# Performance work log

Measured on AMD Instinct MI355X. Metric: run time of the kernel, lower is better.

## Reference

```python
import jax, jax.numpy as jnp
import numpy as np

SPIRAL_LEN = 12
V_LEVELS = [32768, 8192, 2048, 512, 128]
CHANNELS = [3, 32, 64, 128, 256]


def spiral_conv(x, spiral, W, b):
    # x: [B, V, C_in]; spiral: [V, S] neighbor indices
    B, V, C = x.shape
    g = x[:, spiral, :]                      # [B, V, S, C_in] irregular gather
    g = g.reshape(B, V, -1)                  # [B, V, S*C_in]
    return g @ W + b                         # [B, V, C_out]


def mesh_pool(x, idx, w):
    # sparse down_transform (<=3 nnz per row): out[b,i,:] = sum_k w[i,k] * x[b, idx[i,k], :]
    return jnp.einsum('bvkc,vk->bvc', x[:, idx, :], w)


def setup_inputs() -> dict:
    key = jax.random.key(0)
    ks = jax.random.split(key, 32)
    S = SPIRAL_LEN
    V = V_LEVELS
    C = CHANNELS
    d = {}
    d['x'] = jax.random.normal(ks[0], (32, V[0], C[0]), dtype=jnp.float32)
    for i in range(4):
        d[f'spiral{i}'] = jax.random.randint(ks[1 + i], (V[i], S), 0, V[i])
        d[f'didx{i}'] = jax.random.randint(ks[5 + i], (V[i + 1], 3), 0, V[i])
        w = jax.random.uniform(ks[9 + i], (V[i + 1], 3), dtype=jnp.float32)
        d[f'dw{i}'] = w / w.sum(-1, keepdims=True)  # barycentric-like rows
        fan_in = S * C[i]
        d[f'W{i}'] = jax.random.normal(ks[13 + i], (fan_in, C[i + 1]), dtype=jnp.float32) * np.float32(1.0 / np.sqrt(fan_in))
        d[f'b{i}'] = jnp.zeros((C[i + 1],), jnp.float32)
    flat_in = V[4] * C[4]  # num_vert * out_channels[-2]
    d['Wl1'] = jax.random.normal(ks[20], (flat_in, 512), dtype=jnp.float32) * np.float32(1.0 / np.sqrt(flat_in))
    d['bl1'] = jnp.zeros((512,), jnp.float32)
    d['Wl2'] = jax.random.normal(ks[21], (512, 64), dtype=jnp.float32) * np.float32(1.0 / np.sqrt(512))
    d['bl2'] = jnp.zeros((64,), jnp.float32)
    return d


def reference(x, spiral0, spiral1, spiral2, spiral3,
              didx0, didx1, didx2, didx3,
              dw0, dw1, dw2, dw3,
              W0, b0, W1, b1, W2, b2, W3, b3,
              Wl1, bl1, Wl2, bl2):
    spirals = (spiral0, spiral1, spiral2, spiral3)
    didx = (didx0, didx1, didx2, didx3)
    dw = (dw0, dw1, dw2, dw3)
    Wb = ((W0, b0), (W1, b1), (W2, b2), (W3, b3))
    for i in range(4):  # SpiralEnblock: elu(spiral_conv(x)) -> sparse pool
        x = jax.nn.elu(spiral_conv(x, spirals[i], *Wb[i]))
        x = mesh_pool(x, didx[i], dw[i])
    B = x.shape[0]
    x = x.reshape(B, -1)                     # [B, num_vert * C_last]
    x = jax.nn.elu(x @ Wl1 + bl1)            # [B, 512]
    y = x @ Wl2 + bl2                        # [B, latent]
    return (x, y)
```

## Files before the change

### kernel.cpp

```cpp
#include <hip/hip_runtime.h>
#include <cstdint>
#include <cstddef>

typedef _Float16 f16x8 __attribute__((ext_vector_type(8)));
typedef _Float16 f16x4 __attribute__((ext_vector_type(4)));
typedef float f32x4 __attribute__((ext_vector_type(4)));

static __device__ __forceinline__ float elu_f(float t) {
    return t > 0.0f ? t : expm1f(t);
}

typedef __attribute__((address_space(1))) const unsigned int guint;
typedef __attribute__((address_space(3))) unsigned int       luint;
static __device__ __forceinline__ void gload_lds16(const void* g, void* l)
{
    __builtin_amdgcn_global_load_lds((guint*)g, (luint*)l, 16, 0, 0);
}

template<int N>
static __device__ __forceinline__ void vm_wait()
{
    static_assert(N == 0 || N == 4 || N == 5, "vmcnt literal");
    if constexpr (N == 0)      asm volatile("s_waitcnt vmcnt(0)" ::: "memory");
    else if constexpr (N == 4) asm volatile("s_waitcnt vmcnt(4)" ::: "memory");
    else                       asm volatile("s_waitcnt vmcnt(5)" ::: "memory");
    __builtin_amdgcn_sched_barrier(0);
}

static __device__ __forceinline__ int block_pu0(int bid, int P, int vshift_out, int nbl)
{
    if (nbl < 0) return bid * P;
    int xcd  = bid & 7;
    int slot = bid >> 3;
    int nb   = slot & ((1 << nbl) - 1);
    int tile = slot >> nbl;
    return ((xcd + (nb << 3)) << vshift_out) + tile * P;
}

template<int KTOT, int C_OUT, int BN>
__global__ __launch_bounds__(256)
void prep_w(const float* __restrict__ W, _Float16* __restrict__ o)
{
    constexpr int KT = KTOT/64;
    int i = blockIdx.x * 256 + threadIdx.x;
    if (i >= KTOT*C_OUT) return;
    int j = i & 7;
    int rest = i >> 3;
    int n = rest % BN;
    int kc = (rest / BN) & 7;
    int t = (rest / (BN*8)) % KT;
    int y = rest / (BN*8*KT);
    int k = t*64 + kc*8 + j;
    o[i] = (_Float16)W[(size_t)k*C_OUT + y*BN + n];
}

__global__ __launch_bounds__(256)
void prep_w0(const float* __restrict__ W, _Float16* __restrict__ o)
{
    int i = blockIdx.x * 256 + threadIdx.x;
    if (i >= 2048) return;
    int j = i & 7;
    int n = (i >> 3) & 31;
    int kc = i >> 8;
    int k = kc*8 + j;
    int s = k >> 2, c = k & 3;
    float v = (s < 12 && c < 3) ? W[(size_t)(s*3 + c)*32 + n] : 0.0f;
    o[i] = (_Float16)v;
}

__global__ __launch_bounds__(256)
void prep_xT(const float* __restrict__ x, _Float16* __restrict__ xT)
{
    __shared__ _Float16 t[16][64*4 + 8];
    const int v0 = blockIdx.x * 64;
    const int tid = threadIdx.x;
    #pragma unroll
    for (int it = 0; it < 4; ++it) {
        int e = it*256 + tid;
        int b = e >> 6, v = e & 63;
        const float* p = x + ((size_t)b*32768 + v0 + v)*3;
        f16x4 h;
        h[0] = (_Float16)p[0]; h[1] = (_Float16)p[1];
        h[2] = (_Float16)p[2]; h[3] = (_Float16)0.f;
        *(f16x4*)&t[b][v*4] = h;
    }
    __syncthreads();
    #pragma unroll
    for (int it = 0; it < 2; ++it) {
        int e = it*256 + tid;
        int vl = e >> 3, s = e & 7;
        f16x4 a = *(const f16x4*)&t[2*s][vl*4];
        f16x4 b = *(const f16x4*)&t[2*s+1][vl*4];
        f16x8 h;
        h[0]=a[0]; h[1]=a[1]; h[2]=a[2]; h[3]=a[3];
        h[4]=b[0]; h[5]=b[1]; h[6]=b[2]; h[7]=b[3];
        *(f16x8*)&xT[((size_t)(v0+vl)*16 + s*2)*4] = h;
    }
}

__global__ __launch_bounds__(256)
void prep_gidx(const int* __restrict__ didx, const int* __restrict__ spiral,
               unsigned int* __restrict__ g)
{
    int i = blockIdx.x*256 + threadIdx.x;
    if (i >= 24576*8) return;
    int q = i & 7;
    int row = i >> 3;
    unsigned int val = 0;
    if (q < 6) {
        int v = didx[row];
        unsigned int s0 = (unsigned int)spiral[v*12 + q*2];
        unsigned int s1 = (unsigned int)spiral[v*12 + q*2 + 1];
        val = s0 | (s1 << 16);
    }
    g[i] = val;
}

__global__ __launch_bounds__(256)
void conv0T(const _Float16* __restrict__ xT, const unsigned int* __restrict__ gidx,
            const _Float16* __restrict__ Wp, const float* __restrict__ bias,
            const float* __restrict__ dwt, _Float16* __restrict__ out)
{
    __shared__ _Float16 Ep[4][512];
    const int tid  = threadIdx.x;
    const int wave = tid >> 6;
    const int lane = tid & 63;
    const int quad = lane >> 4;
    const int l16  = lane & 15;
    const int u0   = blockIdx.x * 8 + wave * 2;

    f16x8 bf[2][2];
    #pragma unroll
    for (int kt = 0; kt < 2; ++kt)
        #pragma unroll
        for (int nt = 0; nt < 2; ++nt)
            bf[kt][nt] = *(const f16x8*)&Wp[(((kt*4+quad)*32) + nt*16 + l16)*8];
    float bv[2] = { bias[l16], bias[16 + l16] };

    #pragma unroll
    for (int ui = 0; ui < 2; ++ui) {
        int u = u0 + ui;
        f32x4 pacc[2] = {{0.f,0.f,0.f,0.f},{0.f,0.f,0.f,0.f}};
        #pragma unroll
        for (int kp = 0; kp < 3; ++kp) {
            int r = u*3 + kp;
            unsigned int gp0 = gidx[r*8 + quad];
            unsigned int gp1 = gidx[r*8 + 4 + quad];
            f16x4 a0 = *(const f16x4*)&xT[(size_t)(gp0 & 0xffffu)*64 + l16*4];
            f16x4 a1 = *(const f16x4*)&xT[(size_t)(gp0 >> 16)*64 + l16*4];
            f16x4 a2 = *(const f16x4*)&xT[(size_t)(gp1 & 0xffffu)*64 + l16*4];
            f16x4 a3 = *(const f16x4*)&xT[(size_t)(gp1 >> 16)*64 + l16*4];
            f16x8 af0, af1;
            af0[0]=a0[0]; af0[1]=a0[1]; af0[2]=a0[2]; af0[3]=a0[3];
            af0[4]=a1[0]; af0[5]=a1[1]; af0[6]=a1[2]; af0[7]=a1[3];
            af1[0]=a2[0]; af1[1]=a2[1]; af1[2]=a2[2]; af1[3]=a2[3];
            af1[4]=a3[0]; af1[5]=a3[1]; af1[6]=a3[2]; af1[7]=a3[3];
            float dw = dwt[r];
            #pragma unroll
            for (int nt = 0; nt < 2; ++nt) {
                f32x4 m = {0.f,0.f,0.f,0.f};
                m = __builtin_amdgcn_mfma_f32_16x16x32_f16(af0, bf[0][nt], m, 0,0,0);
                m = __builtin_amdgcn_mfma_f32_16x16x32_f16(af1, bf[1][nt], m, 0,0,0);
                #pragma unroll
                for (int rr = 0; rr < 4; ++rr)
                    pacc[nt][rr] += dw * elu_f(m[rr] + bv[nt]);
            }
        }
        #pragma unroll
        for (int nt = 0; nt < 2; ++nt)
            #pragma unroll
            for (int rr = 0; rr < 4; ++rr)
                Ep[wave][(quad*4+rr)*32 + nt*16 + l16] = (_Float16)pacc[nt][rr];
        int b  = lane >> 2;
        int c8 = lane & 3;
        f16x8 rowv = *(const f16x8*)&Ep[wave][b*32 + c8*8];
        *(f16x8*)&out[(size_t)b*262144 + (size_t)u*32 + c8*8] = rowv;
    }
}

template<int C_IN, int C_OUT, int P, int BN, int WGM, int WGN, bool OUT_HALF>
__global__ __launch_bounds__(256)
void conv_pool_mfma(const _Float16* __restrict__ x, const int* __restrict__ spiral,
                    const _Float16* __restrict__ Wp, const float* __restrict__ bias,
                    const int* __restrict__ didx, const float* __restrict__ dwt,
                    void* __restrict__ outv, int vshift_in, int vshift_out, int nbl)
{
    constexpr int R    = 3*P;
    constexpr int KTOT = 12*C_IN;
    constexpr int KT   = KTOT/64;
    constexpr int NST  = KT*2;
    constexpr int WTM  = R/WGM;
    constexpr int WTN  = BN/WGN;
    constexpr int NMT  = WTM/16;
    constexpr int NNT  = WTN/16;
    constexpr int C4   = BN/4;
    constexpr int GS   = (C_IN == 32) ? 1 : 2;
    constexpr int NG   = NST / GS;
    constexpr int CPR  = GS * 4;
    constexpr int CPRS = (CPR == 4) ? 2 : 3;
    constexpr int ACH  = R * CPR;
    constexpr int BCH  = GS * BN * 4;
    constexpr int AIPW = ACH / 256;
    constexpr int BIPW = BCH / 256;
    constexpr int LPW  = AIPW + BIPW;
    constexpr int NBUF = 3;
    constexpr int ASUBH = R * GS * 32;
    constexpr int BSUBH = GS * 32 * BN;
    static_assert(WTM % 16 == 0 && WTN % 16 == 0, "tile");
    static_assert(R <= 256 && (P*C4) % 256 == 0, "loops");
    static_assert(ACH % 256 == 0 && BCH % 256 == 0, "stage");
    static_assert(NST % GS == 0 && GS*32 <= C_IN, "group");
    static_assert(NG >= 3, "pipeline depth");

    constexpr size_t BUFB = (size_t)(NBUF*(ASUBH + BSUBH)) * 2;
    constexpr size_t EB   = (size_t)R * (BN + 4) * 2;
    constexpr size_t GOFF = (BUFB > EB ? BUFB : EB);
    static_assert(GOFF + (size_t)R*12*2 <= 65536, "LDS budget");
    __shared__ __align__(16) char smem[GOFF + (size_t)R*12*2];
    _Float16* Ab = (_Float16*)smem;
    _Float16* Bb = (_Float16*)(smem + (size_t)NBUF*ASUBH*2);
    unsigned short* gidx = (unsigned short*)(smem + GOFF);
    _Float16* E = (_Float16*)smem;

    const int tid  = threadIdx.x;
    const int wave = tid >> 6;
    const int lane = tid & 63;
    const int quad = lane >> 4;
    const int l16  = lane & 15;
    const int wm   = wave / WGN;
    const int wn   = wave % WGN;
    const int pu0  = block_pu0(blockIdx.x, P, vshift_out, nbl);
    const int n0   = blockIdx.y * BN;
    const int vmask_out = (1 << vshift_out) - 1;
    const int base_in = (pu0 >> vshift_out) << vshift_in;

    if (tid < R) {
        int ul = tid / 3;
        int kp = tid - ul*3;
        int u  = (pu0 + ul) & vmask_out;
        int v  = didx[u*3 + kp];
        const int* svp = spiral + v*12;
        #pragma unroll
        for (int j = 0; j < 12; ++j) gidx[tid*12 + j] = (unsigned short)svp[j];
    }
    __syncthreads();

    f32x4 acc[NMT][NNT];
    #pragma unroll
    for (int i = 0; i < NMT; ++i)
        #pragma unroll
        for (int j = 0; j < NNT; ++j) acc[i][j] = (f32x4){0.f, 0.f, 0.f, 0.f};

    const _Float16* xb = x + (size_t)base_in * C_IN;

    auto SWZ = [](int r) -> int {
        return (CPR == 4) ? ((r & 3) ^ ((r >> 2) & 3)) : (r & 7);
    };

    auto stage = [&](int g, int buf) {
        const int k0g = g * GS * 32;
        const int sv  = k0g / C_IN;
        const int c0  = k0g % C_IN;
        _Float16* Ad = Ab + (size_t)buf * ASUBH;
        #pragma unroll
        for (int i = 0; i < AIPW; ++i) {
            int t  = (wave*AIPW + i)*64 + lane;
            int r  = t >> CPRS;
            int q  = t & (CPR - 1);
            int qq = q ^ SWZ(r);
            int gr = gidx[r*12 + sv];
            gload_lds16(xb + (size_t)gr*C_IN + c0 + qq*8,
                        Ad + (size_t)(wave*AIPW + i)*512);
        }
        _Float16* Bd = Bb + (size_t)buf * BSUBH;
        const _Float16* bs = Wp + ((size_t)(blockIdx.y*NST + g*GS)*4)*BN*8;
        #pragma unroll
        for (int i = 0; i < BIPW; ++i) {
            int t = (wave*BIPW + i)*64 + lane;
            gload_lds16(bs + (size_t)t*8,
                        Bd + (size_t)(wave*BIPW + i)*512);
        }
    };

    stage(0, 0);
    stage(1, 1);
    int cur = 0;

    for (int g = 0; g < NG; ++g) {
        if (g + 1 < NG) vm_wait<LPW>(); else vm_wait<0>();
        __builtin_amdgcn_s_barrier();
        __builtin_amdgcn_sched_barrier(0);

        int nx2 = cur + 2; if (nx2 >= NBUF) nx2 -= NBUF;
        if (g + 2 < NG) stage(g + 2, nx2);

        const _Float16* Ar = Ab + (size_t)cur * ASUBH;
        const _Float16* Br = Bb + (size_t)cur * BSUBH;
        #pragma unroll
        for (int sl = 0; sl < GS; ++sl) {
            f16x8 af[NMT], bf[NNT];
            #pragma unroll
            for (int i = 0; i < NMT; ++i) {
                int m = wm*WTM + i*16 + l16;
                af[i] = *(const f16x8*)&Ar[(size_t)(m*CPR + ((sl*4 + quad) ^ SWZ(m)))*8];
            }
            #pragma unroll
            for (int j = 0; j < NNT; ++j) {
                int n = wn*WTN + j*16 + l16;
                bf[j] = *(const f16x8*)&Br[(size_t)((sl*4 + quad)*BN + n)*8];
            }
            #pragma unroll
            for (int i = 0; i < NMT; ++i)
                #pragma unroll
                for (int j = 0; j < NNT; ++j)
                    acc[i][j] = __builtin_amdgcn_mfma_f32_16x16x32_f16(
                        af[i], bf[j], acc[i][j], 0, 0, 0);
        }

        asm volatile("s_waitcnt lgkmcnt(0)" ::: "memory");
        __builtin_amdgcn_sched_barrier(0);
        __builtin_amdgcn_s_barrier();
        __builtin_amdgcn_sched_barrier(0);
        cur = (cur + 1 == NBUF) ? 0 : cur + 1;
    }

    float bv[NNT];
    #pragma unroll
    for (int j = 0; j < NNT; ++j)
        bv[j] = bias[n0 + wn*WTN + j*16 + l16];

    #pragma unroll
    for (int i = 0; i < NMT; ++i) {
        int row_base = wm*WTM + i*16 + quad*4;
        #pragma unroll
        for (int j = 0; j < NNT; ++j) {
            int col = wn*WTN + j*16 + l16;
            #pragma unroll
            for (int r = 0; r < 4; ++r)
                E[(size_t)(row_base + r)*(BN+4) + col] =
                    (_Float16)elu_f(acc[i][j][r] + bv[j]);
        }
    }
    __syncthreads();

    #pragma unroll
    for (int e = tid; e < P*C4; e += 256) {
        int ul = e / C4;
        int c4 = e - ul*C4;
        int pu = pu0 + ul;
        int u  = pu & vmask_out;
        const float* w = dwt + u*3;
        f16x4 a0 = *(const f16x4*)&E[(size_t)(ul*3 + 0)*(BN+4) + c4*4];
        f16x4 a1 = *(const f16x4*)&E[(size_t)(ul*3 + 1)*(BN+4) + c4*4];
        f16x4 a2 = *(const f16x4*)&E[(size_t)(ul*3 + 2)*(BN+4) + c4*4];
        float ox = w[0]*(float)a0[0] + w[1]*(float)a1[0] + w[2]*(float)a2[0];
        float oy = w[0]*(float)a0[1] + w[1]*(float)a1[1] + w[2]*(float)a2[1];
        float oz = w[0]*(float)a0[2] + w[1]*(float)a1[2] + w[2]*(float)a2[2];
        float ow = w[0]*(float)a0[3] + w[1]*(float)a1[3] + w[2]*(float)a2[3];
        if (OUT_HALF) {
            f16x4 h; h[0]=(_Float16)ox; h[1]=(_Float16)oy; h[2]=(_Float16)oz; h[3]=(_Float16)ow;
            *(f16x4*)&((_Float16*)outv)[(size_t)pu*C_OUT + n0 + c4*4] = h;
        } else {
            float4 o; o.x=ox; o.y=oy; o.z=oz; o.w=ow;
            *(float4*)&((float*)outv)[(size_t)pu*C_OUT + n0 + c4*4] = o;
        }
    }
}

__global__ __launch_bounds__(256)
void fc1_partial(const float* __restrict__ xflat, const float* __restrict__ Wl1,
                 float* __restrict__ partial)
{
    __shared__ float sb[8704];
    const int tid = threadIdx.x;
    const int n4 = tid & 31;
    const int kq = (tid >> 5) & 3;
    const int mh = tid >> 7;
    const int nt = blockIdx.x;
    const int ks = blockIdx.y;
    const int kbase = ks * 128;

    for (int e = tid; e < 1024; e += 256) {
        int m = e >> 5, k4 = e & 31;
        *(float4*)&sb[m*128 + k4*4] = *(const float4*)&xflat[(size_t)m*32768 + kbase + k4*4];
    }
    __syncthreads();

    float acc[16][4];
    #pragma unroll
    for (int m = 0; m < 16; ++m)
        #pragma unroll
        for (int c = 0; c < 4; ++c) acc[m][c] = 0.0f;

    const float* Wb = Wl1 + (size_t)(kbase + kq*32)*512 + nt*128 + n4*4;
    #pragma unroll 2
    for (int i = 0; i < 32; i += 4) {
        float4 w0 = *(const float4*)(Wb + (size_t)(i+0)*512);
        float4 w1 = *(const float4*)(Wb + (size_t)(i+1)*512);
        float4 w2 = *(const float4*)(Wb + (size_t)(i+2)*512);
        float4 w3 = *(const float4*)(Wb + (size_t)(i+3)*512);
        #pragma unroll
        for (int m = 0; m < 16; ++m) {
            float4 xv = *(const float4*)&sb[(mh*16 + m)*128 + kq*32 + i];
            acc[m][0] += xv.x*w0.x + xv.y*w1.x + xv.z*w2.x + xv.w*w3.x;
            acc[m][1] += xv.x*w0.y + xv.y*w1.y + xv.z*w2.y + xv.w*w3.y;
            acc[m][2] += xv.x*w0.z + xv.y*w1.z + xv.z*w2.z + xv.w*w3.z;
            acc[m][3] += xv.x*w0.w + xv.y*w1.w + xv.z*w2.w + xv.w*w3.w;
        }
    }
    __syncthreads();

    int slot = (mh*2 + (kq >> 1))*32 + n4;
    if (kq & 1) {
        #pragma unroll
        for (int m = 0; m < 16; ++m)
            *(float4*)&sb[slot*68 + m*4] = *(float4*)&acc[m][0];
    }
    __syncthreads();
    if (!(kq & 1)) {
        #pragma unroll
        for (int m = 0; m < 16; ++m) {
            float4 v = *(const float4*)&sb[slot*68 + m*4];
            acc[m][0] += v.x; acc[m][1] += v.y; acc[m][2] += v.z; acc[m][3] += v.w;
        }
    }
    __syncthreads();
    int slot2 = mh*32 + n4;
    if (kq == 2) {
        #pragma unroll
        for (int m = 0; m < 16; ++m)
            *(float4*)&sb[slot2*68 + m*4] = *(float4*)&acc[m][0];
    }
    __syncthreads();
    if (kq == 0) {
        float* pb = partial + ((size_t)(ks*4 + nt)*32 + mh*16)*128 + n4*4;
        #pragma unroll
        for (int m = 0; m < 16; ++m) {
            float4 v = *(const float4*)&sb[slot2*68 + m*4];
            float4 o;
            o.x = acc[m][0] + v.x; o.y = acc[m][1] + v.y;
            o.z = acc[m][2] + v.z; o.w = acc[m][3] + v.w;
            *(float4*)(pb + (size_t)m*128) = o;
        }
    }
}

__global__ __launch_bounds__(256)
void fc1_reduce(const float* __restrict__ partial, const float* __restrict__ bl1,
                float* __restrict__ hout)
{
    int i = blockIdx.x * 256 + threadIdx.x;
    int m = i >> 9, n = i & 511;
    int nt = n >> 7, nl = n & 127;
    const float* p = partial + ((size_t)nt*32 + m)*128 + nl;
    float s = 0.0f;
    #pragma unroll 8
    for (int ks = 0; ks < 256; ++ks)
        s += p[(size_t)ks*4*4096];
    hout[i] = elu_f(s + bl1[n]);
}

__global__ __launch_bounds__(64)
void fc2_kernel(const float* __restrict__ h, const float* __restrict__ Wl2,
                const float* __restrict__ bl2, float* __restrict__ y)
{
    int m = blockIdx.x;
    int n = threadIdx.x;
    float s = bl2[n];
    for (int k = 0; k < 512; ++k)
        s += h[(size_t)m*512 + k] * Wl2[(size_t)k*64 + n];
    y[(size_t)m*64 + n] = s;
}

extern "C" void kernel_launch(void* const* d_in, const int* in_sizes, int n_in,
                              void* d_out, int out_size, void* d_ws, size_t ws_size,
                              hipStream_t stream)
{
    (void)in_sizes; (void)n_in; (void)out_size; (void)ws_size;

    const float* x0 = (const float*)d_in[0];
    const int*   sp[4]; const int* didx[4]; const float* dwp[4];
    const float* Wp[4]; const float* bp[4];
    for (int i = 0; i < 4; ++i) {
        sp[i]   = (const int*)  d_in[1 + i*5 + 0];
        didx[i] = (const int*)  d_in[1 + i*5 + 1];
        dwp[i]  = (const float*)d_in[1 + i*5 + 2];
        Wp[i]   = (const float*)d_in[1 + i*5 + 3];
        bp[i]   = (const float*)d_in[1 + i*5 + 4];
    }
    const float* Wl1 = (const float*)d_in[21];
    const float* bl1 = (const float*)d_in[22];
    const float* Wl2 = (const float*)d_in[23];
    const float* bl2 = (const float*)d_in[24];
    float* out = (float*)d_out;

    char* wsb = (char*)d_ws;
    float* persist      = (float*)wsb;
    float* partial      = (float*)(wsb + (4<<20));
    _Float16* xT        = (_Float16*)(wsb + (24<<20));
    _Float16* pooled0   = (_Float16*)(wsb + (32<<20));
    _Float16* pooled1   = (_Float16*)(wsb + (48<<20));
    _Float16* pooled2   = (_Float16*)(wsb + (56<<20));
    unsigned int* gidx0 = (unsigned int*)(wsb + (60<<20));
    _Float16* w0h       = (_Float16*)(wsb + (61<<20));
    _Float16* w1h       = w0h + 2048;
    _Float16* w2h       = w1h + 24576;
    _Float16* w3h       = w2h + 98304;

    prep_w0<<<8, 256, 0, stream>>>(Wp[0], w0h);
    prep_w< 384,  64,  64><<<( 24576 + 255)/256, 256, 0, stream>>>(Wp[1], w1h);
    prep_w< 768, 128,  64><<<( 98304 + 255)/256, 256, 0, stream>>>(Wp[2], w2h);
    prep_w<1536, 256,  64><<<(393216 + 255)/256, 256, 0, stream>>>(Wp[3], w3h);
    prep_gidx<<<768, 256, 0, stream>>>(didx[0], sp[0], gidx0);

    for (int h = 0; h < 2; ++h) {
        _Float16* xTh = xT + (size_t)h*2097152;
        prep_xT<<<512, 256, 0, stream>>>(x0 + (size_t)h*16*98304, xTh);
        conv0T<<<1024, 256, 0, stream>>>(xTh, gidx0, w0h, bp[0], dwp[0],
                                         pooled0 + (size_t)h*16*262144);
    }

    conv_pool_mfma<32,64,64,64,4,1,true><<<1024, 256, 0, stream>>>(
        pooled0, sp[1], w1h, bp[1], didx[1], dwp[1], pooled1, 13, 11, 2);

    conv_pool_mfma<64,128,32,64,2,2,true><<<dim3(512, 2), 256, 0, stream>>>(
        pooled1, sp[2], w2h, bp[2], didx[2], dwp[2], pooled2, 11, 9, 2);

    conv_pool_mfma<128,256,32,64,2,2,false><<<dim3(128, 4), 256, 0, stream>>>(
        pooled2, sp[3], w3h, bp[3], didx[3], dwp[3], persist, 9, 7, 2);

    fc1_partial<<<dim3(4, 256), 256, 0, stream>>>(persist, Wl1, partial);
    fc1_reduce<<<64, 256, 0, stream>>>(partial, bl1, out);

    fc2_kernel<<<32, 64, 0, stream>>>(out, Wl2, bl2, out + 16384);
}
```

Before: 302.0 us.

## Merge prep kernels into one launch and use double buffering for conv1

The four weight-prep kernels and the gather-index prep are fused into a single prep_all kernel that dispatches on block id. The two-half loops over prep_xT and conv0T are folded into single launches with twice the grid, so several small launches and their gaps go away. conv_pool_mfma gains an NBUF template parameter, and the first layer switches to a 2-buffer pipeline. That lowers LDS use and may raise occupancy, but leaves less prefetch depth to hide load latency.

```diff
diff --git a/kernel.cpp b/kernel.cpp
--- a/kernel.cpp
+++ b/kernel.cpp
@@ -38,12 +38,10 @@
 }
 
 template<int KTOT, int C_OUT, int BN>
-__global__ __launch_bounds__(256)
-void prep_w(const float* __restrict__ W, _Float16* __restrict__ o)
+static __device__ __forceinline__ void prep_w_body(const float* __restrict__ W,
+                                                   _Float16* __restrict__ o, int i)
 {
     constexpr int KT = KTOT/64;
-    int i = blockIdx.x * 256 + threadIdx.x;
-    if (i >= KTOT*C_OUT) return;
     int j = i & 7;
     int rest = i >> 3;
     int n = rest % BN;
@@ -55,34 +53,63 @@
 }
 
 __global__ __launch_bounds__(256)
-void prep_w0(const float* __restrict__ W, _Float16* __restrict__ o)
-{
-    int i = blockIdx.x * 256 + threadIdx.x;
-    if (i >= 2048) return;
-    int j = i & 7;
-    int n = (i >> 3) & 31;
-    int kc = i >> 8;
-    int k = kc*8 + j;
-    int s = k >> 2, c = k & 3;
-    float v = (s < 12 && c < 3) ? W[(size_t)(s*3 + c)*32 + n] : 0.0f;
-    o[i] = (_Float16)v;
+void prep_all(const float* __restrict__ W0, const float* __restrict__ W1,
+              const float* __restrict__ W2, const float* __restrict__ W3,
+              const int* __restrict__ didx0, const int* __restrict__ spiral0,
+              _Float16* __restrict__ w0h, _Float16* __restrict__ w1h,
+              _Float16* __restrict__ w2h, _Float16* __restrict__ w3h,
+              unsigned int* __restrict__ g)
+{
+    const int bid = blockIdx.x;
+    const int tid = threadIdx.x;
+    if (bid < 8) {
+        int i = bid*256 + tid;
+        int j = i & 7;
+        int n = (i >> 3) & 31;
+        int kc = i >> 8;
+        int k = kc*8 + j;
+        int s = k >> 2, c = k & 3;
+        float v = (s < 12 && c < 3) ? W0[(size_t)(s*3 + c)*32 + n] : 0.0f;
+        w0h[i] = (_Float16)v;
+    } else if (bid < 104) {
+        prep_w_body< 384,  64, 64>(W1, w1h, (bid - 8)*256 + tid);
+    } else if (bid < 488) {
+        prep_w_body< 768, 128, 64>(W2, w2h, (bid - 104)*256 + tid);
+    } else if (bid < 2024) {
+        prep_w_body<1536, 256, 64>(W3, w3h, (bid - 488)*256 + tid);
+    } else {
+        int i = (bid - 2024)*256 + tid;
+        int q = i & 7;
+        int row = i >> 3;
+        unsigned int val = 0;
+        if (q < 6) {
+            int v = didx0[row];
+            unsigned int s0 = (unsigned int)spiral0[v*12 + q*2];
+            unsigned int s1 = (unsigned int)spiral0[v*12 + q*2 + 1];
+            val = s0 | (s1 << 16);
+        }
+        g[i] = val;
+    }
 }
 
 __global__ __launch_bounds__(256)
-void prep_xT(const float* __restrict__ x, _Float16* __restrict__ xT)
+void prep_xT(const float* __restrict__ x0, _Float16* __restrict__ xT)
 {
     __shared__ _Float16 t[16][64*4 + 8];
-    const int v0 = blockIdx.x * 64;
+    const int h  = blockIdx.x >> 9;
+    const float* x = x0 + (size_t)h*16*98304;
+    _Float16* xTh  = xT + (size_t)h*2097152;
+    const int v0 = (blockIdx.x & 511) * 64;
     const int tid = threadIdx.x;
     #pragma unroll
     for (int it = 0; it < 4; ++it) {
         int e = it*256 + tid;
         int b = e >> 6, v = e & 63;
         const float* p = x + ((size_t)b*32768 + v0 + v)*3;
-        f16x4 h;
-        h[0] = (_Float16)p[0]; h[1] = (_Float16)p[1];
-        h[2] = (_Float16)p[2]; h[3] = (_Float16)0.f;
-        *(f16x4*)&t[b][v*4] = h;
+        f16x4 hh;
+        hh[0] = (_Float16)p[0]; hh[1] = (_Float16)p[1];
+        hh[2] = (_Float16)p[2]; hh[3] = (_Float16)0.f;
+        *(f16x4*)&t[b][v*4] = hh;
     }
     __syncthreads();
     #pragma unroll
@@ -91,43 +118,28 @@
         int vl = e >> 3, s = e & 7;
         f16x4 a = *(const f16x4*)&t[2*s][vl*4];
         f16x4 b = *(const f16x4*)&t[2*s+1][vl*4];
-        f16x8 h;
-        h[0]=a[0]; h[1]=a[1]; h[2]=a[2]; h[3]=a[3];
-        h[4]=b[0]; h[5]=b[1]; h[6]=b[2]; h[7]=b[3];
-        *(f16x8*)&xT[((size_t)(v0+vl)*16 + s*2)*4] = h;
+        f16x8 hh;
+        hh[0]=a[0]; hh[1]=a[1]; hh[2]=a[2]; hh[3]=a[3];
+        hh[4]=b[0]; hh[5]=b[1]; hh[6]=b[2]; hh[7]=b[3];
+        *(f16x8*)&xTh[((size_t)(v0+vl)*16 + s*2)*4] = hh;
     }
 }
 
 __global__ __launch_bounds__(256)
-void prep_gidx(const int* __restrict__ didx, const int* __restrict__ spiral,
-               unsigned int* __restrict__ g)
-{
-    int i = blockIdx.x*256 + threadIdx.x;
-    if (i >= 24576*8) return;
-    int q = i & 7;
-    int row = i >> 3;
-    unsigned int val = 0;
-    if (q < 6) {
-        int v = didx[row];
-        unsigned int s0 = (unsigned int)spiral[v*12 + q*2];
-        unsigned int s1 = (unsigned int)spiral[v*12 + q*2 + 1];
-        val = s0 | (s1 << 16);
-    }
-    g[i] = val;
-}
-
-__global__ __launch_bounds__(256)
-void conv0T(const _Float16* __restrict__ xT, const unsigned int* __restrict__ gidx,
+void conv0T(const _Float16* __restrict__ xT0, const unsigned int* __restrict__ gidx,
             const _Float16* __restrict__ Wp, const float* __restrict__ bias,
-            const float* __restrict__ dwt, _Float16* __restrict__ out)
+            const float* __restrict__ dwt, _Float16* __restrict__ out0)
 {
     __shared__ _Float16 Ep[4][512];
+    const int h = blockIdx.x >> 10;
+    const _Float16* xT = xT0 + (size_t)h*2097152;
+    _Float16* out = out0 + (size_t)h*16*262144;
     const int tid  = threadIdx.x;
     const int wave = tid >> 6;
     const int lane = tid & 63;
     const int quad = lane >> 4;
     const int l16  = lane & 15;
-    const int u0   = blockIdx.x * 8 + wave * 2;
+    const int u0   = (blockIdx.x & 1023) * 8 + wave * 2;
 
     f16x8 bf[2][2];
     #pragma unroll
@@ -178,7 +190,7 @@
     }
 }
 
-template<int C_IN, int C_OUT, int P, int BN, int WGM, int WGN, bool OUT_HALF>
+template<int C_IN, int C_OUT, int P, int BN, int WGM, int WGN, bool OUT_HALF, int NBUF>
 __global__ __launch_bounds__(256)
 void conv_pool_mfma(const _Float16* __restrict__ x, const int* __restrict__ spiral,
                     const _Float16* __restrict__ Wp, const float* __restrict__ bias,
@@ -203,14 +215,14 @@
     constexpr int AIPW = ACH / 256;
     constexpr int BIPW = BCH / 256;
     constexpr int LPW  = AIPW + BIPW;
-    constexpr int NBUF = 3;
     constexpr int ASUBH = R * GS * 32;
     constexpr int BSUBH = GS * 32 * BN;
     static_assert(WTM % 16 == 0 && WTN % 16 == 0, "tile");
     static_assert(R <= 256 && (P*C4) % 256 == 0, "loops");
     static_assert(ACH % 256 == 0 && BCH % 256 == 0, "stage");
     static_assert(NST % GS == 0 && GS*32 <= C_IN, "group");
-    static_assert(NG >= 3, "pipeline depth");
+    static_assert(NBUF == 2 || NBUF == 3, "nbuf");
+    static_assert(NBUF == 2 ? NG >= 2 : NG >= 3, "pipeline depth");
 
     constexpr size_t BUFB = (size_t)(NBUF*(ASUBH + BSUBH)) * 2;
     constexpr size_t EB   = (size_t)R * (BN + 4) * 2;
@@ -282,20 +294,9 @@
         }
     };
 
-    stage(0, 0);
-    stage(1, 1);
-    int cur = 0;
-
-    for (int g = 0; g < NG; ++g) {
-        if (g + 1 < NG) vm_wait<LPW>(); else vm_wait<0>();
-        __builtin_amdgcn_s_barrier();
-        __builtin_amdgcn_sched_barrier(0);
-
-        int nx2 = cur + 2; if (nx2 >= NBUF) nx2 -= NBUF;
-        if (g + 2 < NG) stage(g + 2, nx2);
-
-        const _Float16* Ar = Ab + (size_t)cur * ASUBH;
-        const _Float16* Br = Bb + (size_t)cur * BSUBH;
+    auto compute = [&](int cb) {
+        const _Float16* Ar = Ab + (size_t)cb * ASUBH;
+        const _Float16* Br = Bb + (size_t)cb * BSUBH;
         #pragma unroll
         for (int sl = 0; sl < GS; ++sl) {
             f16x8 af[NMT], bf[NNT];
@@ -316,12 +317,44 @@
                     acc[i][j] = __builtin_amdgcn_mfma_f32_16x16x32_f16(
                         af[i], bf[j], acc[i][j], 0, 0, 0);
         }
-
-        asm volatile("s_waitcnt lgkmcnt(0)" ::: "memory");
-        __builtin_amdgcn_sched_barrier(0);
-        __builtin_amdgcn_s_barrier();
-        __builtin_amdgcn_sched_barrier(0);
-        cur = (cur + 1 == NBUF) ? 0 : cur + 1;
+    };
+
+    if constexpr (NBUF == 3) {
+        stage(0, 0);
+        stage(1, 1);
+        int cur = 0;
+        for (int g = 0; g < NG; ++g) {
+            if (g + 1 < NG) vm_wait<LPW>(); else vm_wait<0>();
+            __builtin_amdgcn_s_barrier();
+            __builtin_amdgcn_sched_barrier(0);
+            int nx2 = cur + 2; if (nx2 >= 3) nx2 -= 3;
+            if (g + 2 < NG) stage(g + 2, nx2);
+            compute(cur);
+            asm volatile("s_waitcnt lgkmcnt(0)" ::: "memory");
+            __builtin_amdgcn_sched_barrier(0);
+            __builtin_amdgcn_s_barrier();
+            __builtin_amdgcn_sched_barrier(0);
+            cur = (cur + 1 == 3) ? 0 : cur + 1;
+        }
+    } else {
+        stage(0, 0);
+        int cur = 0;
+        for (int g = 0; g < NG; ++g) {
+            if (g + 1 < NG) {
+                stage(g + 1, cur ^ 1);
+                vm_wait<LPW>();
+            } else {
+                vm_wait<0>();
+            }
+            __builtin_amdgcn_s_barrier();
+            __builtin_amdgcn_sched_barrier(0);
+            compute(cur);
+            asm volatile("s_waitcnt lgkmcnt(0)" ::: "memory");
+            __builtin_amdgcn_sched_barrier(0);
+            __builtin_amdgcn_s_barrier();
+            __builtin_amdgcn_sched_barrier(0);
+            cur ^= 1;
+        }
     }
 
     float bv[NNT];
@@ -507,26 +540,20 @@
     _Float16* w2h       = w1h + 24576;
     _Float16* w3h       = w2h + 98304;
 
-    prep_w0<<<8, 256, 0, stream>>>(Wp[0], w0h);
-    prep_w< 384,  64,  64><<<( 24576 + 255)/256, 256, 0, stream>>>(Wp[1], w1h);
-    prep_w< 768, 128,  64><<<( 98304 + 255)/256, 256, 0, stream>>>(Wp[2], w2h);
-    prep_w<1536, 256,  64><<<(393216 + 255)/256, 256, 0, stream>>>(Wp[3], w3h);
-    prep_gidx<<<768, 256, 0, stream>>>(didx[0], sp[0], gidx0);
-
-    for (int h = 0; h < 2; ++h) {
-        _Float16* xTh = xT + (size_t)h*2097152;
-        prep_xT<<<512, 256, 0, stream>>>(x0 + (size_t)h*16*98304, xTh);
-        conv0T<<<1024, 256, 0, stream>>>(xTh, gidx0, w0h, bp[0], dwp[0],
-                                         pooled0 + (size_t)h*16*262144);
-    }
-
-    conv_pool_mfma<32,64,64,64,4,1,true><<<1024, 256, 0, stream>>>(
+    prep_all<<<2792, 256, 0, stream>>>(Wp[0], Wp[1], Wp[2], Wp[3],
+                                       didx[0], sp[0],
+                                       w0h, w1h, w2h, w3h, gidx0);
+
+    prep_xT<<<1024, 256, 0, stream>>>(x0, xT);
+    conv0T<<<2048, 256, 0, stream>>>(xT, gidx0, w0h, bp[0], dwp[0], pooled0);
+
+    conv_pool_mfma<32,64,64,64,4,1,true,2><<<1024, 256, 0, stream>>>(
         pooled0, sp[1], w1h, bp[1], didx[1], dwp[1], pooled1, 13, 11, 2);
 
-    conv_pool_mfma<64,128,32,64,2,2,true><<<dim3(512, 2), 256, 0, stream>>>(
+    conv_pool_mfma<64,128,32,64,2,2,true,3><<<dim3(512, 2), 256, 0, stream>>>(
         pooled1, sp[2], w2h, bp[2], didx[2], dwp[2], pooled2, 11, 9, 2);
 
-    conv_pool_mfma<128,256,32,64,2,2,false><<<dim3(128, 4), 256, 0, stream>>>(
+    conv_pool_mfma<128,256,32,64,2,2,false,3><<<dim3(128, 4), 256, 0, stream>>>(
         pooled2, sp[3], w3h, bp[3], didx[3], dwp[3], persist, 9, 7, 2);
 
     fc1_partial<<<dim3(4, 256), 256, 0, stream>>>(persist, Wl1, partial);
```

New measurement: 283.8 us. -6.0%, faster.
